# Kernel optimization log

Hardware: AMD Instinct MI355X
Metric: run time of the kernel (lower is better)

## Reference

```python
import jax, jax.numpy as jnp
import numpy as np


def haar_level(x):
    """One 2D Haar (periodization-equivalent for even sizes) DWT on [B,K,C,H,W].
    Returns [B,4K,C,H/2,W/2] with per-parent band order (LL, Hx, Hy, Hxy),
    matching the tree's append order yl, yh0, yh1, yh2."""
    B, K, C, H, W = x.shape
    x = x.reshape(B, K, C, H // 2, 2, W // 2, 2)
    a = x[:, :, :, :, 0, :, 0]
    b = x[:, :, :, :, 0, :, 1]
    c = x[:, :, :, :, 1, :, 0]
    d = x[:, :, :, :, 1, :, 1]
    ll = (a + b + c + d) * 0.5
    h1 = (a - b + c - d) * 0.5   # high along width
    h2 = (a + b - c - d) * 0.5   # high along height
    h3 = (a - b - c + d) * 0.5   # diagonal
    out = jnp.stack([ll, h1, h2, h3], axis=2)  # [B,K,4,C,H/2,W/2]
    return out.reshape(B, 4 * K, C, H // 2, W // 2)


def conv2d(x, w, b, stride, pad):
    y = jax.lax.conv_general_dilated(
        x, w, window_strides=(stride, stride),
        padding=[(pad, pad), (pad, pad)],
        dimension_numbers=('NCHW', 'OIHW', 'NCHW'))
    return y + b[None, :, None, None]


def setup_inputs() -> dict:
    key = jax.random.key(0)
    ks = jax.random.split(key, 9)
    s = 0.05
    return {
        'x':        jax.random.normal(ks[0], (64, 3, 224, 224), dtype=jnp.float32),
        'w_s1':     jax.random.normal(ks[1], (192, 3, 7, 7), dtype=jnp.float32) * s,
        'b_s1':     jax.random.normal(ks[2], (192,), dtype=jnp.float32) * s,
        'w_s2':     jax.random.normal(ks[3], (192, 192, 7, 7), dtype=jnp.float32) * s,
        'b_s2':     jax.random.normal(ks[4], (192,), dtype=jnp.float32) * s,
        'w_p':      jax.random.normal(ks[5], (768, 960, 3, 3), dtype=jnp.float32) * s,
        'b_p':      jax.random.normal(ks[6], (768,), dtype=jnp.float32) * s,
        'cls_token': jax.random.normal(ks[7], (1, 1, 768), dtype=jnp.float32),
        'positions': jax.random.normal(ks[8], (50, 768), dtype=jnp.float32),
    }


def reference(x, w_s1, b_s1, w_s2, b_s2, w_p, b_p, cls_token, positions):
    B = x.shape[0]
    # ---- 4-level full Haar wavelet packet tree (vectorized over subbands) ----
    t = x[:, None]                      # [B,1,3,224,224]
    for _ in range(4):
        t = haar_level(t)               # -> [B,256,3,14,14]
    wav = t.reshape(B, 256 * 3, 14, 14)  # [B,768,14,14] (tree concat order)
    # ---- spatial branch: two strided 7x7 convs (224 -> 56 -> 14) ----
    sp = conv2d(x, w_s1, b_s1, stride=4, pad=3)
    sp = conv2d(sp, w_s2, b_s2, stride=4, pad=3)   # [B,192,14,14]
    feat = jnp.concatenate([wav, sp], axis=1)      # [B,960,14,14]
    # ---- patch projection conv 3x3 s2 -> 7x7, flatten to tokens ----
    y = conv2d(feat, w_p, b_p, stride=2, pad=1)    # [B,768,7,7]
    y = y.reshape(B, 768, 49).transpose(0, 2, 1)   # [B,49,768]
    cls = jnp.broadcast_to(cls_token, (B, 1, 768))
    y = jnp.concatenate([cls, y], axis=1) + positions  # [B,50,768]
    return y
```

## Files before the change

### kernel.cpp

```cpp
#include <hip/hip_runtime.h>
#include <stdint.h>

typedef __attribute__((ext_vector_type(8))) short short8;
typedef __attribute__((ext_vector_type(4))) float floatx4;

__device__ inline unsigned short f2bf(float f){
  union { float fv; unsigned int u; } v; v.fv = f;
  unsigned int u = v.u;
  unsigned int r = ((u >> 16) & 1u) + 0x7FFFu;
  return (unsigned short)((u + r) >> 16);
}

__device__ __forceinline__ void async16(const void* g, void* l){
  __builtin_amdgcn_global_load_lds(
      (const __attribute__((address_space(1))) unsigned int*)g,
      (__attribute__((address_space(3))) unsigned int*)l, 16, 0, 0);
}

__global__ void prep_w1(const float* __restrict__ w, unsigned short* __restrict__ w1p){
  int i = blockIdx.x*256 + threadIdx.x;
  if (i >= 192*192) return;
  int k = i % 192, o = i / 192;
  int cc = k >> 3, kx = k & 7;
  unsigned short v = 0;
  if (cc < 21 && kx < 7){
    int c = cc / 7, ky = cc % 7;
    v = f2bf(w[(o*3 + c)*49 + ky*7 + kx]);
  }
  w1p[i] = v;
}
__global__ void prep_w2(const float* __restrict__ w, unsigned short* __restrict__ w2p){
  int i = blockIdx.x*256 + threadIdx.x;
  if (i >= 192*9408) return;
  int k = i % 9408, o = i / 9408;
  int g = k / 192, c = k % 192;
  int ky = g / 7, kx = g % 7;
  w2p[i] = f2bf(w[((o*192 + c)*7 + ky)*7 + kx]);
}
__global__ void prep_w3(const float* __restrict__ w, unsigned short* __restrict__ w3p){
  int i = blockIdx.x*256 + threadIdx.x;
  if (i >= 768*8640) return;
  int k = i % 8640, o = i / 8640;
  int g = k / 960, c = k % 960;
  int ky = g / 3, kx = g % 3;
  w3p[i] = f2bf(w[((o*960 + c)*3 + ky)*3 + kx]);
}
__global__ void prep_zp(unsigned int* __restrict__ zp){
  zp[threadIdx.x] = 0u;
}

__global__ void pad_x2(const float* __restrict__ x, unsigned short* __restrict__ xh2){
  int idx = blockIdx.x*256 + threadIdx.x;
  if (idx >= 64*3*230*56*8) return;
  int kx = idx & 7; int t = idx >> 3;
  int ox = t % 56;  t /= 56;
  int iy = t % 230; t /= 230;
  int row = iy - 3;
  int col = 4*ox - 3 + kx;
  unsigned short v = 0;
  if (row >= 0 && row < 224 && col >= 0 && col < 224)
    v = f2bf(x[((size_t)t*224 + row)*224 + col]);
  xh2[idx] = v;
}

__global__ void wavelet_kernel(const float* __restrict__ x, unsigned short* __restrict__ feat){
  int blk = blockIdx.x;
  int j = blk % 14; blk /= 14;
  int i = blk % 14; blk /= 14;
  int c = blk % 3;  int b = blk / 3;
  int t = threadIdx.x;
  int u = t >> 4, v = t & 15;
  float val = x[((size_t)(b*3 + c)*224 + (i*16 + u))*224 + (j*16 + v)];
  #pragma unroll
  for (int bit = 1; bit < 64; bit <<= 1){
    float p = __shfl_xor(val, bit);
    val = (t & bit) ? (p - val) : (val + p);
  }
  __shared__ float s[256];
  #pragma unroll
  for (int bit = 64; bit < 256; bit <<= 1){
    s[t] = val; __syncthreads();
    float p = s[t ^ bit]; __syncthreads();
    val = (t & bit) ? (p - val) : (val + p);
  }
  s[t] = val; __syncthreads();
  int k = t;
  int d1 = (k>>6)&3, d2 = (k>>4)&3, d3 = (k>>2)&3, d4 = k&3;
  int mr = (d1>>1) | ((d2>>1)<<1) | ((d3>>1)<<2) | ((d4>>1)<<3);
  int mc = (d1&1)  | ((d2&1)<<1)  | ((d3&1)<<2)  | ((d4&1)<<3);
  float outv = s[mr*16 + mc] * 0.0625f;
  feat[((size_t)((b*14 + i)*14 + j))*960 + (k*3 + c)] = f2bf(outv);
}

__global__ __launch_bounds__(256) void conv1_gemm(const unsigned short* __restrict__ xh2,
                                                  const unsigned short* __restrict__ w1p,
                                                  const float* __restrict__ b1,
                                                  unsigned short* __restrict__ sp1){
  __shared__ unsigned short As[2][128*64], Bs[2][64*64];
  int m0 = blockIdx.x*128, n0 = blockIdx.y*64;
  int tid = threadIdx.x, wave = tid >> 6, lane = tid & 63;
  int l16 = lane & 15, quad = lane >> 4;
  int wy = wave >> 1, wx = wave & 1;
  int r8 = lane >> 3, kb = (lane & 7) ^ r8;

  int Abase[4];
  #pragma unroll
  for (int j = 0; j < 4; j++){
    int row = wave*32 + j*8 + r8;
    int m = m0 + row;
    int ox = m % 56; int t = m / 56; int oy = t % 56; int b = t / 56;
    Abase[j] = (b*690 + 4*oy)*448 + ox*8;
  }
  const unsigned short* pB0 = w1p + (n0 + wave*16 + r8)*192 + kb*8;
  const unsigned short* pB1 = pB0 + 8*192;

  int sw = l16 & 7;
  int xo0 = ((quad    ) ^ sw)*8;
  int xo1 = ((quad + 4) ^ sw)*8;
  int aoff[4];
  #pragma unroll
  for (int mt = 0; mt < 4; mt++) aoff[mt] = (wy*64 + mt*16 + l16)*64;
  int boff0 = (wx*32 + l16)*64, boff1 = boff0 + 16*64;

  floatx4 acc[4][2];
  #pragma unroll
  for (int mt = 0; mt < 4; mt++)
    #pragma unroll
    for (int nt = 0; nt < 2; nt++) acc[mt][nt] = (floatx4){0.f,0.f,0.f,0.f};

  auto stage = [&](int i, int buf){
    int cc = i*8 + kb;
    int c = (cc*147) >> 10;
    int ky = cc - 7*c;
    int koff = (c*230 + ky)*448;
    #pragma unroll
    for (int j = 0; j < 4; j++)
      async16(xh2 + Abase[j] + koff, (void*)&As[buf][(wave*32 + j*8)*64]);
    async16(pB0 + i*64, (void*)&Bs[buf][(wave*16    )*64]);
    async16(pB1 + i*64, (void*)&Bs[buf][(wave*16 + 8)*64]);
  };

  stage(0, 0);
  __syncthreads();
  #pragma unroll
  for (int i = 0; i < 3; i++){
    int buf = i & 1;
    if (i < 2) stage(i+1, buf ^ 1);
    #pragma unroll
    for (int ks = 0; ks < 2; ks++){
      int xo = ks ? xo1 : xo0;
      short8 b0 = *(const short8*)&Bs[buf][boff0 + xo];
      short8 b1 = *(const short8*)&Bs[buf][boff1 + xo];
      #pragma unroll
      for (int mt = 0; mt < 4; mt++){
        short8 a = *(const short8*)&As[buf][aoff[mt] + xo];
        acc[mt][0] = __builtin_amdgcn_mfma_f32_16x16x32_bf16(a, b0, acc[mt][0], 0, 0, 0);
        acc[mt][1] = __builtin_amdgcn_mfma_f32_16x16x32_bf16(a, b1, acc[mt][1], 0, 0, 0);
      }
    }
    __syncthreads();
  }

  #pragma unroll
  for (int mt = 0; mt < 4; mt++){
    #pragma unroll
    for (int rg = 0; rg < 4; rg++){
      int row = wy*64 + mt*16 + quad*4 + rg;
      size_t ob = (size_t)(m0 + row)*192;
      #pragma unroll
      for (int nt = 0; nt < 2; nt++){
        int nn = n0 + wx*32 + nt*16 + l16;
        sp1[ob + nn] = f2bf(acc[mt][nt][rg] + b1[nn]);
      }
    }
  }
}

template<int MODE>
__global__ __launch_bounds__(256) void conv_gemm(const unsigned short* __restrict__ Ain,
                                                 const unsigned short* __restrict__ Bt,
                                                 const float* __restrict__ bias,
                                                 const float* __restrict__ pos,
                                                 const unsigned short* __restrict__ zp,
                                                 void* __restrict__ outp){
  constexpr int OH  = (MODE==2) ? 14 : 7;
  constexpr int OW  = OH;
  constexpr int IH  = (MODE==2) ? 56 : 14;
  constexpr int IW  = IH;
  constexpr int Cin = (MODE==2) ? 192 : 960;
  constexpr int KW  = (MODE==2) ? 7 : 3;
  constexpr int S   = (MODE==2) ? 4 : 2;
  constexpr int P   = (MODE==2) ? 3 : 1;
  constexpr int K   = (MODE==2) ? 9408 : 8640;
  constexpr int NSTEP = K/32;
  constexpr int MTI = (MODE==2) ? 196 : 49;
  constexpr int GRP = (MODE==2) ? 24 : 96;

  int id = blockIdx.x;
  int g = id / GRP, rem = id % GRP;
  int mtile = g*8 + (rem & 7), ntile = rem >> 3;
  if (mtile >= MTI) return;
  int m0 = mtile*64, n0 = ntile*64;

  __shared__ unsigned short smem[32768];

  int tid = threadIdx.x, wave = tid >> 6, lane = tid & 63;
  int l16 = lane & 15, quad = lane >> 4;

  unsigned short* wbase = &smem[wave*8192];

  int s0 = (NSTEP*wave) >> 2;
  int s1 = (NSTEP*(wave+1)) >> 2;
  int n = s1 - s0;

  int k32 = s0*32;
  int c0 = k32 % Cin;
  int gk = k32 / Cin;
  int kx = gk % KW, ky = gk / KW;

  int rsub = lane >> 2;
  int soff = ((lane & 3) ^ (rsub & 3)) * 8;

  int Abase[4], iyb[4], ixb[4];
  const unsigned short* pB[4];
  #pragma unroll
  for (int j = 0; j < 4; j++){
    int R = 16*j + rsub;
    int m = m0 + R;
    int ox = m % OW; int t = m / OW; int oy = t % OH; int b = t / OH;
    iyb[j] = S*oy - P; ixb[j] = S*ox - P;
    Abase[j] = ((b*IH + iyb[j])*IW + ixb[j])*Cin;
    pB[j] = Bt + (size_t)(n0 + R)*K + k32 + soff;
  }

  int fro = l16*32 + ((quad ^ (l16 & 3)) * 8);

  floatx4 acc[4][4];
  #pragma unroll
  for (int mi = 0; mi < 4; mi++)
    #pragma unroll
    for (int ni = 0; ni < 4; ni++) acc[mi][ni] = (floatx4){0.f,0.f,0.f,0.f};

  auto stage = [&](int buf){
    int koff = (ky*IW + kx)*Cin + c0;
    #pragma unroll
    for (int j = 0; j < 4; j++){
      int iy = iyb[j] + ky, ix = ixb[j] + kx;
      bool v = ((unsigned)iy < (unsigned)IH) & ((unsigned)ix < (unsigned)IW);
      const unsigned short* src = v ? (Ain + Abase[j] + koff + soff) : (zp + soff);
      async16(src, (void*)(wbase + buf*2048 + j*512));
    }
    #pragma unroll
    for (int j = 0; j < 4; j++){
      async16(pB[j], (void*)(wbase + 4096 + buf*2048 + j*512));
      pB[j] += 32;
    }
    c0 += 32;
    if (c0 == Cin){ c0 = 0; kx++; if (kx == KW){ kx = 0; ky++; } }
  };

  auto compute = [&](int buf){
    const unsigned short* Ab = wbase + buf*2048;
    const unsigned short* Bb = wbase + 4096 + buf*2048;
    short8 a[4], b[4];
    #pragma unroll
    for (int i = 0; i < 4; i++){
      a[i] = *(const short8*)&Ab[fro + i*512];
      b[i] = *(const short8*)&Bb[fro + i*512];
    }
    #pragma unroll
    for (int mi = 0; mi < 4; mi++)
      #pragma unroll
      for (int ni = 0; ni < 4; ni++)
        acc[mi][ni] = __builtin_amdgcn_mfma_f32_16x16x32_bf16(a[mi], b[ni], acc[mi][ni], 0, 0, 0);
  };

  stage(0); stage(1);
  for (int i = 0; i < n-2; i++){
    asm volatile("s_waitcnt vmcnt(8)" ::: "memory");
    compute(i & 1);
    asm volatile("s_waitcnt lgkmcnt(0)" ::: "memory");
    stage(i & 1);
  }
  asm volatile("s_waitcnt vmcnt(8)" ::: "memory");
  compute(n & 1);
  asm volatile("s_waitcnt vmcnt(0)" ::: "memory");
  compute((n-1) & 1);

  asm volatile("s_waitcnt lgkmcnt(0) vmcnt(0)" ::: "memory");
  __builtin_amdgcn_sched_barrier(0);
  float* red = (float*)wbase;
  #pragma unroll
  for (int mi = 0; mi < 4; mi++)
    #pragma unroll
    for (int ni = 0; ni < 4; ni++)
      #pragma unroll
      for (int rg = 0; rg < 4; rg++){
        int row = mi*16 + quad*4 + rg;
        int col = ni*16 + l16;
        red[row*64 + col] = acc[mi][ni][rg];
      }
  __syncthreads();
  const float* r0 = (const float*)&smem[0];
  const float* r1 = (const float*)&smem[8192];
  const float* r2 = (const float*)&smem[16384];
  const float* r3 = (const float*)&smem[24576];
  #pragma unroll
  for (int j = 0; j < 16; j++){
    int e = tid + 256*j;
    float v = r0[e] + r1[e] + r2[e] + r3[e];
    int col = e & 63, row = e >> 6;
    int mm = m0 + row, nn = n0 + col;
    v += bias[nn];
    if (MODE == 2){
      ((unsigned short*)outp)[(size_t)mm*960 + 768 + nn] = f2bf(v);
    } else {
      int b2 = mm / 49;
      int tt = mm - b2*49;
      v += pos[(size_t)(1 + tt)*768 + nn];
      ((float*)outp)[((size_t)(mm + b2 + 1))*768 + nn] = v;
    }
  }
}

__global__ void cls_kernel(const float* __restrict__ cls, const float* __restrict__ pos,
                           float* __restrict__ out){
  int i = blockIdx.x*256 + threadIdx.x;
  if (i >= 64*768) return;
  int e = i % 768, b = i / 768;
  out[(size_t)(b*50)*768 + e] = cls[e] + pos[e];
}

extern "C" void kernel_launch(void* const* d_in, const int* in_sizes, int n_in,
                              void* d_out, int out_size, void* d_ws, size_t ws_size,
                              hipStream_t stream){
  (void)in_sizes; (void)n_in; (void)out_size;
  const float* x    = (const float*)d_in[0];
  const float* w_s1 = (const float*)d_in[1];
  const float* b_s1 = (const float*)d_in[2];
  const float* w_s2 = (const float*)d_in[3];
  const float* b_s2 = (const float*)d_in[4];
  const float* w_p  = (const float*)d_in[5];
  const float* b_p  = (const float*)d_in[6];
  const float* cls  = (const float*)d_in[7];
  const float* pos  = (const float*)d_in[8];
  float* out = (float*)d_out;

  char* ws = (char*)d_ws;
  if (ws_size < 118235136u) return;
  unsigned short* w1p  = (unsigned short*)(ws + 0);
  unsigned short* sp1  = (unsigned short*)(ws + 131072);
  unsigned short* zp   = (unsigned short*)(ws + 77201408u);
  unsigned short* w2p  = (unsigned short*)(ws + 77266944u);
  unsigned short* w3p  = (unsigned short*)(ws + 80879616u);
  unsigned short* feat = (unsigned short*)(ws + 94150656u);
  unsigned short* xh2  = (unsigned short*)(ws + 77266944u);

  prep_w1<<<(192*192 + 255)/256, 256, 0, stream>>>(w_s1, w1p);
  pad_x2<<<(64*3*230*56*8)/256, 256, 0, stream>>>(x, xh2);
  conv1_gemm<<<dim3(1568, 3), 256, 0, stream>>>(xh2, w1p, b_s1, sp1);
  prep_w2<<<(192*9408 + 255)/256, 256, 0, stream>>>(w_s2, w2p);
  prep_w3<<<(768*8640 + 255)/256, 256, 0, stream>>>(w_p, w3p);
  prep_zp<<<1, 64, 0, stream>>>((unsigned int*)zp);
  wavelet_kernel<<<64*3*14*14, 256, 0, stream>>>(x, feat);
  conv_gemm<2><<<600, 256, 0, stream>>>(sp1, w2p, b_s2, nullptr, zp, (void*)feat);
  conv_gemm<3><<<672, 256, 0, stream>>>(feat, w3p, b_p, pos, zp, (void*)out);
  cls_kernel<<<(64*768 + 255)/256, 256, 0, stream>>>(cls, pos, out);
}
```

Measured before the change: 484.7 us.

## Stage K in shared 128-wide chunks across waves with block barriers

Replaces per-wave private split-K pipelines with a block-cooperative scheme. All four waves jointly load 128-wide K chunks of A and B into a double-buffered shared tile, and each wave computes its own 32-wide slice of every chunk. The hand-tuned vmcnt waits are replaced by a __syncthreads per chunk, and im2col addresses are now computed per 16-byte load with bounds checks for the K tail. This aims to give more regular, coalesced loads and a simpler pipeline, at the cost of block-wide barriers and extra integer div/mod per stage.

```diff
diff --git a/kernel.cpp b/kernel.cpp
--- a/kernel.cpp
+++ b/kernel.cpp
@@ -192,7 +192,7 @@
   constexpr int S   = (MODE==2) ? 4 : 2;
   constexpr int P   = (MODE==2) ? 3 : 1;
   constexpr int K   = (MODE==2) ? 9408 : 8640;
-  constexpr int NSTEP = K/32;
+  constexpr int NMEGA = (K + 127)/128;
   constexpr int MTI = (MODE==2) ? 196 : 49;
   constexpr int GRP = (MODE==2) ? 24 : 96;
 
@@ -204,36 +204,26 @@
 
   __shared__ unsigned short smem[32768];
 
-  int tid = threadIdx.x, wave = tid >> 6, lane = tid & 63;
+  int tid = threadIdx.x, wv = tid >> 6, lane = tid & 63;
   int l16 = lane & 15, quad = lane >> 4;
 
-  unsigned short* wbase = &smem[wave*8192];
-
-  int s0 = (NSTEP*wave) >> 2;
-  int s1 = (NSTEP*(wave+1)) >> 2;
-  int n = s1 - s0;
-
-  int k32 = s0*32;
-  int c0 = k32 % Cin;
-  int gk = k32 / Cin;
-  int kx = gk % KW, ky = gk / KW;
-
-  int rsub = lane >> 2;
-  int soff = ((lane & 3) ^ (rsub & 3)) * 8;
-
-  int Abase[4], iyb[4], ixb[4];
-  const unsigned short* pB[4];
+  int lr = lane >> 4;
+  int gp = lane & 15;
+  int ksoff[4], abase[4], iyb[4], ixb[4];
+  const unsigned short* bptr[4];
   #pragma unroll
   for (int j = 0; j < 4; j++){
-    int R = 16*j + rsub;
-    int m = m0 + R;
-    int ox = m % OW; int t = m / OW; int oy = t % OH; int b = t / OH;
+    int r = wv*16 + j*4 + lr;
+    int gsrc = gp ^ (r & 7);
+    ksoff[j] = gsrc*8;
+    int m = m0 + r;
+    int ox = m % OW; int t = m / OW; int oy = t % OH; int bb = t / OH;
     iyb[j] = S*oy - P; ixb[j] = S*ox - P;
-    Abase[j] = ((b*IH + iyb[j])*IW + ixb[j])*Cin;
-    pB[j] = Bt + (size_t)(n0 + R)*K + k32 + soff;
-  }
-
-  int fro = l16*32 + ((quad ^ (l16 & 3)) * 8);
+    abase[j] = ((bb*IH + iyb[j])*IW + ixb[j])*Cin;
+    bptr[j] = Bt + (size_t)(n0 + r)*K + ksoff[j];
+  }
+
+  int fro = l16*128 + ((4*wv + quad) ^ (l16 & 7))*8;
 
   floatx4 acc[4][4];
   #pragma unroll
@@ -241,32 +231,36 @@
     #pragma unroll
     for (int ni = 0; ni < 4; ni++) acc[mi][ni] = (floatx4){0.f,0.f,0.f,0.f};
 
-  auto stage = [&](int buf){
-    int koff = (ky*IW + kx)*Cin + c0;
+  auto stage = [&](int buf, int k0){
+    unsigned short* Ad = &smem[buf*8192];
+    unsigned short* Bd = &smem[16384 + buf*8192];
     #pragma unroll
     for (int j = 0; j < 4; j++){
+      int k = k0 + ksoff[j];
+      int c = k % Cin;
+      int tp = k / Cin;
+      int ky = tp / KW, kx = tp - ky*KW;
       int iy = iyb[j] + ky, ix = ixb[j] + kx;
-      bool v = ((unsigned)iy < (unsigned)IH) & ((unsigned)ix < (unsigned)IW);
-      const unsigned short* src = v ? (Ain + Abase[j] + koff + soff) : (zp + soff);
-      async16(src, (void*)(wbase + buf*2048 + j*512));
+      bool v = ((unsigned)iy < (unsigned)IH) & ((unsigned)ix < (unsigned)IW) & (k < K);
+      const unsigned short* src = v ? (Ain + abase[j] + (ky*IW + kx)*Cin + c) : zp;
+      async16(src, (void*)&Ad[(wv*16 + j*4)*128]);
     }
     #pragma unroll
     for (int j = 0; j < 4; j++){
-      async16(pB[j], (void*)(wbase + 4096 + buf*2048 + j*512));
-      pB[j] += 32;
-    }
-    c0 += 32;
-    if (c0 == Cin){ c0 = 0; kx++; if (kx == KW){ kx = 0; ky++; } }
+      int k = k0 + ksoff[j];
+      const unsigned short* src = (k < K) ? (bptr[j] + k0) : zp;
+      async16(src, (void*)&Bd[(wv*16 + j*4)*128]);
+    }
   };
 
   auto compute = [&](int buf){
-    const unsigned short* Ab = wbase + buf*2048;
-    const unsigned short* Bb = wbase + 4096 + buf*2048;
+    const unsigned short* Ab = &smem[buf*8192];
+    const unsigned short* Bb = &smem[16384 + buf*8192];
     short8 a[4], b[4];
     #pragma unroll
     for (int i = 0; i < 4; i++){
-      a[i] = *(const short8*)&Ab[fro + i*512];
-      b[i] = *(const short8*)&Bb[fro + i*512];
+      a[i] = *(const short8*)&Ab[fro + i*2048];
+      b[i] = *(const short8*)&Bb[fro + i*2048];
     }
     #pragma unroll
     for (int mi = 0; mi < 4; mi++)
@@ -275,21 +269,16 @@
         acc[mi][ni] = __builtin_amdgcn_mfma_f32_16x16x32_bf16(a[mi], b[ni], acc[mi][ni], 0, 0, 0);
   };
 
-  stage(0); stage(1);
-  for (int i = 0; i < n-2; i++){
-    asm volatile("s_waitcnt vmcnt(8)" ::: "memory");
-    compute(i & 1);
-    asm volatile("s_waitcnt lgkmcnt(0)" ::: "memory");
-    stage(i & 1);
-  }
-  asm volatile("s_waitcnt vmcnt(8)" ::: "memory");
-  compute(n & 1);
-  asm volatile("s_waitcnt vmcnt(0)" ::: "memory");
-  compute((n-1) & 1);
-
-  asm volatile("s_waitcnt lgkmcnt(0) vmcnt(0)" ::: "memory");
-  __builtin_amdgcn_sched_barrier(0);
-  float* red = (float*)wbase;
+  stage(0, 0);
+  __syncthreads();
+  for (int i = 0; i < NMEGA; i++){
+    int buf = i & 1;
+    if (i + 1 < NMEGA) stage(buf ^ 1, (i+1)*128);
+    compute(buf);
+    __syncthreads();
+  }
+
+  float* red = (float*)&smem[wv * 8192];
   #pragma unroll
   for (int mi = 0; mi < 4; mi++)
     #pragma unroll
```

Result: no change. 483.2 us (-0.3%).
